# Kernel optimization log

Measured on AMD Instinct MI355X. Metric: run time of the kernel, lower is better.

Reference implementation:

```python
import jax, jax.numpy as jnp
import numpy as np

B, S, DIM, H, HD = 2, 2048, 512, 8, 64
VD = DIM // H  # 64
QK = H * HD


def setup_inputs() -> dict:
    key = jax.random.key(0)
    k1, k2, k3, k4, k5 = jax.random.split(key, 5)
    x = jax.random.normal(k1, (B, S, DIM), dtype=jnp.float32)
    mask = jax.random.bernoulli(k2, 0.5, (B, S))
    # per-position rotation matrices, scaled to keep activations O(1)
    rotator = jax.random.normal(k3, (B, S, HD, HD), dtype=jnp.float32) / np.sqrt(HD)
    # torch Linear weights: [out_features, in_features], no bias
    W_trans = jax.random.normal(k4, (2 * QK + DIM, DIM), dtype=jnp.float32) / np.sqrt(DIM)
    W_o = jax.random.normal(k5, (DIM, DIM), dtype=jnp.float32) / np.sqrt(DIM)
    return {"x": x, "mask": mask, "rotator": rotator, "W_trans": W_trans, "W_o": W_o}


def _taylor_attention(qs, ks, vs, mask):
    # 2nd-order Taylor approximation of exp for softmax weights
    # qs/ks: [B,S,H,HD], vs: [B,S,H,VD], mask: [B,S] key mask
    scores = jnp.einsum('bqhd,bkhd->bhqk', qs, ks) / np.sqrt(HD)
    w = 1.0 + scores + 0.5 * scores * scores
    w = jnp.where(mask[:, None, None, :], w, 0.0)
    w = w / jnp.sum(w, axis=-1, keepdims=True)
    out = jnp.einsum('bhqk,bkhd->bqhd', w, vs)
    return out.reshape(out.shape[0], out.shape[1], -1)  # [B,S,DIM]


def reference(x, mask, rotator, W_trans, W_o):
    t = x @ W_trans.T  # [B,S,2*QK+DIM]
    qs = t[..., :QK].reshape(B, S, H, HD)
    ks = t[..., QK:2 * QK].reshape(B, S, H, HD)
    vs = t[..., 2 * QK:].reshape(B, S, H, VD)
    sel = mask[..., None, None]
    qs = jnp.where(sel, jnp.einsum('bsij,bshj->bshi', rotator, qs), qs)
    ks = jnp.where(sel, jnp.einsum('bsij,bshj->bshi', rotator, ks), ks)
    out = _taylor_attention(qs, ks, vs, mask)
    return out @ W_o.T
```

## Files before the change

### kernel.cpp

```cpp
#include <hip/hip_runtime.h>
#include <hip/hip_bf16.h>

#define B_    2
#define S_    2048
#define DIM_  512
#define H_    8
#define HD_   64
#define TOUT_ 1536
#define ROWS_ (B_ * S_)

typedef unsigned short ushort_t;
typedef __attribute__((ext_vector_type(8))) __bf16 bf16x8;
typedef __attribute__((ext_vector_type(4))) float floatx4;

#define AS_GLB __attribute__((address_space(1)))
#define AS_LDS __attribute__((address_space(3)))

__device__ __forceinline__ float bf2f(unsigned int u) { return __uint_as_float(u << 16); }
__device__ __forceinline__ unsigned short f2bfu(float f) {
    unsigned u = __float_as_uint(f);
    unsigned r = (u + 0x7fffu + ((u >> 16) & 1u)) >> 16;
    return (unsigned short)r;
}
__device__ __forceinline__ bf16x8 cvt8(const float* p) {
    float4 a = *reinterpret_cast<const float4*>(p);
    float4 b = *reinterpret_cast<const float4*>(p + 4);
    ushort_t o[8] = {f2bfu(a.x), f2bfu(a.y), f2bfu(a.z), f2bfu(a.w),
                     f2bfu(b.x), f2bfu(b.y), f2bfu(b.z), f2bfu(b.w)};
    return *reinterpret_cast<bf16x8*>(o);
}

__global__ void tmha_detect(const unsigned char* mb, int* flags) {
    __shared__ int s_bf, s_f, s_u8;
    int tid = threadIdx.x;
    if (tid == 0) { s_bf = 0; s_f = 0; s_u8 = 0; }
    __syncthreads();
    int cbf = 0, cf = 0, cu8 = 0;
    for (int i = tid; i < 4096; i += 256) {
        unsigned char v = mb[i];
        if (v == 0x3F || v == 0x80) {
            cf++;
            if ((i & 3) == 1) cbf++;
        } else if (v != 0 && (i & 3) != 0) {
            cu8++;
        }
    }
    atomicAdd(&s_bf, cbf); atomicAdd(&s_f, cf); atomicAdd(&s_u8, cu8);
    __syncthreads();
    if (tid == 0) {
        int mcls;
        if (s_bf > 0)      mcls = 2;
        else if (s_f > 0)  mcls = 3;
        else if (s_u8 > 0) mcls = 0;
        else               mcls = 1;
        flags[1] = mcls;
    }
}

__global__ void tmha_decode_mask(const unsigned char* mb, const int* flags, int* wm) {
    int i = blockIdx.x * 256 + threadIdx.x;
    if (i >= ROWS_) return;
    int cls = flags[1];
    int v;
    if (cls == 0)      v = (mb[i] != 0);
    else if (cls == 1) v = (reinterpret_cast<const int*>(mb)[i] != 0);
    else if (cls == 2) v = ((reinterpret_cast<const unsigned short*>(mb)[i] & 0x7fffu) != 0);
    else               v = ((reinterpret_cast<const unsigned int*>(mb)[i] & 0x7fffffffu) != 0);
    wm[i] = v;
}

__global__ __launch_bounds__(256) void cast_bf16(const float* __restrict__ src,
                                                 ushort_t* __restrict__ dst, int n4) {
    int i = blockIdx.x * 256 + threadIdx.x;
    if (i >= n4) return;
    float4 v = reinterpret_cast<const float4*>(src)[i];
    ushort_t o[4] = {f2bfu(v.x), f2bfu(v.y), f2bfu(v.z), f2bfu(v.w)};
    reinterpret_cast<uint2*>(dst)[i] = *reinterpret_cast<uint2*>(o);
}

template <int TM, int N, int K, bool OUT_BF16>
__global__ __launch_bounds__(256) void mfma_gemm_bt(const ushort_t* __restrict__ A,
                                                    const ushort_t* __restrict__ Bm,
                                                    void* __restrict__ Cout) {
    constexpr int FM = TM / 32;
    __shared__ __align__(16) ushort_t As[TM * 64];
    __shared__ __align__(16) ushort_t Bs[128 * 64];
    int tid = threadIdx.x;
    int lane = tid & 63;
    int wv = tid >> 6;
    int wm = wv >> 1, wn = wv & 1;
    int quad = lane >> 4;
    int mrow = lane & 15;
    int bx = blockIdx.x;
    int by = blockIdx.y;

    floatx4 acc[FM][4];
#pragma unroll
    for (int i = 0; i < FM; i++)
#pragma unroll
        for (int j = 0; j < 4; j++) acc[i][j] = (floatx4){0.f, 0.f, 0.f, 0.f};

    for (int k0 = 0; k0 < K; k0 += 64) {
#pragma unroll
        for (int t = 0; t < TM / 32; t++) {
            int p = (wv * (TM / 32) + t) * 64 + lane;
            int row = p >> 3, cp = p & 7;
            int gc = cp ^ (row & 7);
            const ushort_t* ga = A + (size_t)(by * TM + row) * K + k0 + gc * 8;
            __builtin_amdgcn_global_load_lds((const AS_GLB unsigned int*)ga,
                                             (AS_LDS unsigned int*)&As[(size_t)(wv * (TM / 32) + t) * 64 * 8],
                                             16, 0, 0);
        }
#pragma unroll
        for (int t = 0; t < 4; t++) {
            int p = (wv * 4 + t) * 64 + lane;
            int row = p >> 3, cp = p & 7;
            int gc = cp ^ (row & 7);
            const ushort_t* gb = Bm + (size_t)(bx * 128 + row) * K + k0 + gc * 8;
            __builtin_amdgcn_global_load_lds((const AS_GLB unsigned int*)gb,
                                             (AS_LDS unsigned int*)&Bs[(size_t)(wv * 4 + t) * 64 * 8],
                                             16, 0, 0);
        }
        __syncthreads();
#pragma unroll
        for (int ks = 0; ks < 64; ks += 32) {
            int c = (ks >> 3) + quad;
            bf16x8 af[FM], bf[4];
#pragma unroll
            for (int i = 0; i < FM; i++) {
                int row = wm * (TM / 2) + i * 16 + mrow;
                int pos = row * 8 + (c ^ (row & 7));
                af[i] = *reinterpret_cast<const bf16x8*>(&As[pos * 8]);
            }
#pragma unroll
            for (int j = 0; j < 4; j++) {
                int row = wn * 64 + j * 16 + mrow;
                int pos = row * 8 + (c ^ (row & 7));
                bf[j] = *reinterpret_cast<const bf16x8*>(&Bs[pos * 8]);
            }
#pragma unroll
            for (int i = 0; i < FM; i++)
#pragma unroll
                for (int j = 0; j < 4; j++)
                    acc[i][j] = __builtin_amdgcn_mfma_f32_16x16x32_bf16(af[i], bf[j], acc[i][j], 0, 0, 0);
        }
        __syncthreads();
    }

    int col0 = bx * 128 + wn * 64 + mrow;
    int row0 = by * TM + wm * (TM / 2) + quad * 4;
    if constexpr (OUT_BF16) {
        ushort_t* C = reinterpret_cast<ushort_t*>(Cout);
#pragma unroll
        for (int i = 0; i < FM; i++)
#pragma unroll
            for (int j = 0; j < 4; j++)
#pragma unroll
                for (int r = 0; r < 4; r++)
                    C[(size_t)(row0 + i * 16 + r) * N + col0 + j * 16] = f2bfu(acc[i][j][r]);
    } else {
        float* C = reinterpret_cast<float*>(Cout);
#pragma unroll
        for (int i = 0; i < FM; i++)
#pragma unroll
            for (int j = 0; j < 4; j++)
#pragma unroll
                for (int r = 0; r < 4; r++)
                    C[(size_t)(row0 + i * 16 + r) * N + col0 + j * 16] = acc[i][j][r];
    }
}

__global__ __launch_bounds__(256) void rot_qk_mfma(const ushort_t* __restrict__ t,
                                                   const float* __restrict__ rotG,
                                                   const int* __restrict__ wm,
                                                   ushort_t* __restrict__ Qb,
                                                   ushort_t* __restrict__ Kb) {
    int lane = threadIdx.x & 63;
    int wv = threadIdx.x >> 6;
    int row = blockIdx.x * 4 + wv;
    int b = row >> 11, s = row & 2047;
    int lm = lane & 15, quad = lane >> 4;
    const ushort_t* trow = t + (size_t)row * TOUT_;

    if (wm[row]) {
        bf16x8 af[2];
#pragma unroll
        for (int kc = 0; kc < 2; kc++)
            af[kc] = *reinterpret_cast<const bf16x8*>(trow + lm * 64 + kc * 32 + quad * 8);

        const float* R = rotG + (size_t)row * 4096;
        floatx4 dacc[4];
#pragma unroll
        for (int nb = 0; nb < 4; nb++) dacc[nb] = (floatx4){0.f, 0.f, 0.f, 0.f};
#pragma unroll
        for (int nb = 0; nb < 4; nb++)
#pragma unroll
            for (int kc = 0; kc < 2; kc++) {
                bf16x8 bfr = cvt8(R + (size_t)(nb * 16 + lm) * 64 + kc * 32 + quad * 8);
                dacc[nb] = __builtin_amdgcn_mfma_f32_16x16x32_bf16(af[kc], bfr, dacc[nb], 0, 0, 0);
            }
#pragma unroll
        for (int nb = 0; nb < 4; nb++)
#pragma unroll
            for (int r = 0; r < 4; r++) {
                int vec = quad * 4 + r;
                int h = vec & 7;
                ushort_t* dst = (vec >= 8 ? Kb : Qb);
                dst[((size_t)(b * 8 + h) * 2048 + s) * 64 + nb * 16 + lm] = f2bfu(dacc[nb][r]);
            }
    } else {
#pragma unroll
        for (int nb = 0; nb < 4; nb++)
#pragma unroll
            for (int r = 0; r < 4; r++) {
                int vec = quad * 4 + r;
                int h = vec & 7;
                ushort_t* dst = (vec >= 8 ? Kb : Qb);
                dst[((size_t)(b * 8 + h) * 2048 + s) * 64 + nb * 16 + lm] = trow[vec * 64 + nb * 16 + lm];
            }
    }
}

__global__ __launch_bounds__(256) void prep_vt(const ushort_t* __restrict__ t,
                                               const int* __restrict__ wm,
                                               ushort_t* __restrict__ VtG) {
    __shared__ ushort_t tile[64][72];
    __shared__ float mrow[64];
    int st = blockIdx.x;
    int bh = blockIdx.y;
    int b = bh >> 3, h = bh & 7;
    int tid = threadIdx.x;
    if (tid < 64) mrow[tid] = wm[b * 2048 + st * 64 + tid] ? 1.0f : 0.0f;
#pragma unroll
    for (int i = 0; i < 2; i++) {
        int q = i * 256 + tid;
        int r = q >> 3, c8 = (q & 7) * 8;
        uint4 v = *reinterpret_cast<const uint4*>(
            t + (size_t)(b * 2048 + st * 64 + r) * TOUT_ + 1024 + h * 64 + c8);
        *reinterpret_cast<uint4*>(&tile[r][c8]) = v;
    }
    __syncthreads();
#pragma unroll
    for (int i = 0; i < 8; i++) {
        int e = i * 256 + tid;
        int d = e >> 5, sl = (e & 31) * 2;
        unsigned u0 = (mrow[sl]     != 0.f) ? (unsigned)tile[sl][d]     : 0u;
        unsigned u1 = (mrow[sl + 1] != 0.f) ? (unsigned)tile[sl + 1][d] : 0u;
        *reinterpret_cast<unsigned int*>(VtG + ((size_t)bh * 65 + d) * 2048 + st * 64 + sl) = u0 | (u1 << 16);
    }
    if (tid < 32) {
        int sl = tid * 2;
        unsigned m0 = mrow[sl]     != 0.f ? 0x3F80u : 0u;
        unsigned m1 = mrow[sl + 1] != 0.f ? 0x3F80u : 0u;
        *reinterpret_cast<unsigned int*>(VtG + ((size_t)bh * 65 + 64) * 2048 + st * 64 + sl) = m0 | (m1 << 16);
    }
}

__global__ __launch_bounds__(256) void tmha_attn_mfma(const ushort_t* __restrict__ Qb,
                                                      const ushort_t* __restrict__ Kb,
                                                      const ushort_t* __restrict__ VtG,
                                                      float* __restrict__ numer,
                                                      float* __restrict__ den) {
    __shared__ __align__(16) ushort_t Ks[512 * 8];
    __shared__ __align__(16) ushort_t Vs[520 * 8];
    __shared__ __align__(16) ushort_t Ps[512 * 8];
    int tid = threadIdx.x;
    int lane = tid & 63;
    int wv = tid >> 6;
    int lm = lane & 15;
    int quad = lane >> 4;
    int qt = blockIdx.x;
    int h = blockIdx.y;
    int z = blockIdx.z;
    int b = z >> 1;
    int ks = z & 1;
    int bh = b * 8 + h;

    bf16x8 qf[2];
    {
        const ushort_t* qp = Qb + ((size_t)bh * 2048 + qt * 64 + wv * 16 + lm) * 64 + quad * 8;
        qf[0] = *reinterpret_cast<const bf16x8*>(qp);
        qf[1] = *reinterpret_cast<const bf16x8*>(qp + 32);
    }

    bf16x8 vzero;
    *reinterpret_cast<uint4*>(&vzero) = (uint4){0u, 0u, 0u, 0u};

    floatx4 oacc[5];
#pragma unroll
    for (int j = 0; j < 5; j++) oacc[j] = (floatx4){0.f, 0.f, 0.f, 0.f};

    for (int kt = ks * 1024; kt < ks * 1024 + 1024; kt += 64) {
#pragma unroll
        for (int t4 = 0; t4 < 2; t4++) {
            int p = (wv * 2 + t4) * 64 + lane;
            int row = p >> 3, cp = p & 7;
            int gc = cp ^ (row & 7);
            const ushort_t* g = Kb + ((size_t)bh * 2048 + kt + row) * 64 + gc * 8;
            __builtin_amdgcn_global_load_lds((const AS_GLB unsigned int*)g,
                                             (AS_LDS unsigned int*)&Ks[(size_t)(wv * 2 + t4) * 64 * 8],
                                             16, 0, 0);
        }
#pragma unroll
        for (int t4 = 0; t4 < 2; t4++) {
            int p = (wv * 2 + t4) * 64 + lane;
            int row = p >> 3, cp = p & 7;
            int gc = cp ^ (row & 7);
            const ushort_t* g = VtG + ((size_t)bh * 65 + row) * 2048 + kt + gc * 8;
            __builtin_amdgcn_global_load_lds((const AS_GLB unsigned int*)g,
                                             (AS_LDS unsigned int*)&Vs[(size_t)(wv * 2 + t4) * 64 * 8],
                                             16, 0, 0);
        }
        if (tid < 8) {
            const ushort_t* g = VtG + ((size_t)bh * 65 + 64) * 2048 + kt + tid * 8;
            __builtin_amdgcn_global_load_lds((const AS_GLB unsigned int*)g,
                                             (AS_LDS unsigned int*)&Vs[512 * 8],
                                             16, 0, 0);
        }
        __syncthreads();

        floatx4 sacc[4];
#pragma unroll
        for (int j = 0; j < 4; j++) sacc[j] = (floatx4){0.f, 0.f, 0.f, 0.f};
#pragma unroll
        for (int j = 0; j < 4; j++) {
            int row = j * 16 + lm;
#pragma unroll
            for (int kc = 0; kc < 2; kc++) {
                int c = kc * 4 + quad;
                int pos = row * 8 + (c ^ (row & 7));
                bf16x8 bk = *reinterpret_cast<const bf16x8*>(&Ks[pos * 8]);
                sacc[j] = __builtin_amdgcn_mfma_f32_16x16x32_bf16(qf[kc], bk, sacc[j], 0, 0, 0);
            }
        }

#pragma unroll
        for (int j = 0; j < 4; j++)
#pragma unroll
            for (int r = 0; r < 4; r++) {
                float s = sacc[j][r];
                float wgt = fmaf(s, fmaf(s, 0.0078125f, 0.125f), 1.0f);
                int m = wv * 16 + quad * 4 + r;
                int col = j * 16 + lm;
                int cw = col >> 3;
                int pos = m * 8 + (cw ^ (m & 7));
                Ps[pos * 8 + (col & 7)] = f2bfu(wgt);
            }
        asm volatile("s_waitcnt lgkmcnt(0)" ::: "memory");

        int qrow_l = wv * 16 + lm;
#pragma unroll
        for (int j = 0; j < 5; j++) {
            int vrow = (j < 4) ? (j * 16 + lm) : 64;
#pragma unroll
            for (int kc = 0; kc < 2; kc++) {
                int c = kc * 4 + quad;
                int ppos = qrow_l * 8 + (c ^ (qrow_l & 7));
                bf16x8 pa = *reinterpret_cast<const bf16x8*>(&Ps[ppos * 8]);
                int vpos = vrow * 8 + (c ^ (vrow & 7));
                bf16x8 vb = *reinterpret_cast<const bf16x8*>(&Vs[vpos * 8]);
                if (j == 4 && lm != 0) vb = vzero;
                oacc[j] = __builtin_amdgcn_mfma_f32_16x16x32_bf16(pa, vb, oacc[j], 0, 0, 0);
            }
        }
        __syncthreads();
    }

#pragma unroll
    for (int j = 0; j < 4; j++)
#pragma unroll
        for (int r = 0; r < 4; r++) {
            int qrow = b * 2048 + qt * 64 + wv * 16 + quad * 4 + r;
            numer[((size_t)ks * ROWS_ + qrow) * DIM_ + h * 64 + j * 16 + lm] = oacc[j][r];
        }
    if (lm == 0) {
#pragma unroll
        for (int r = 0; r < 4; r++) {
            int qrow = b * 2048 + qt * 64 + wv * 16 + quad * 4 + r;
            den[((size_t)ks * ROWS_ + qrow) * 8 + h] = oacc[4][r];
        }
    }
}

__global__ __launch_bounds__(256) void attn_combine(const float* __restrict__ numer,
                                                    const float* __restrict__ den,
                                                    ushort_t* __restrict__ attnAb) {
    int i = blockIdx.x * 256 + threadIdx.x;
    int row = i >> 7;
    int c4 = (i & 127) * 4;
    int h = c4 >> 6;
    float4 n0 = *reinterpret_cast<const float4*>(&numer[(size_t)row * DIM_ + c4]);
    float4 n1 = *reinterpret_cast<const float4*>(&numer[((size_t)ROWS_ + row) * DIM_ + c4]);
    float d = den[(size_t)row * 8 + h] + den[((size_t)ROWS_ + row) * 8 + h];
    float inv = 1.0f / d;
    ushort_t o[4] = {f2bfu((n0.x + n1.x) * inv), f2bfu((n0.y + n1.y) * inv),
                     f2bfu((n0.z + n1.z) * inv), f2bfu((n0.w + n1.w) * inv)};
    *reinterpret_cast<uint2*>(&attnAb[(size_t)row * DIM_ + c4]) = *reinterpret_cast<uint2*>(o);
}

extern "C" void kernel_launch(void* const* d_in, const int* in_sizes, int n_in,
                              void* d_out, int out_size, void* d_ws, size_t ws_size,
                              hipStream_t stream) {
    (void)in_sizes; (void)n_in; (void)out_size; (void)ws_size;
    const float* x    = (const float*)d_in[0];
    const void*  mask = d_in[1];
    const float* rot  = (const float*)d_in[2];
    const float* Wt   = (const float*)d_in[3];
    const float* Wo   = (const float*)d_in[4];

    char* ws = (char*)d_ws;
    int* flags       = (int*)ws;
    int* wmask       = (int*)(ws + 64);
    ushort_t* t      = (ushort_t*)(ws + 32768);
    ushort_t* Xb     = (ushort_t*)(ws + 25198592);
    ushort_t* Wtb    = (ushort_t*)(ws + 29392896);
    ushort_t* Wob    = (ushort_t*)(ws + 30965760);
    ushort_t* Qb     = (ushort_t*)(ws + 31490048);
    ushort_t* Kb     = (ushort_t*)(ws + 35684352);
    ushort_t* VtG    = (ushort_t*)(ws + 39878656);
    ushort_t* attnAb = (ushort_t*)(ws + 44138496);
    float* numer     = (float*)(ws + 32768);
    float* den       = (float*)(ws + 32768 + 16777216);

    tmha_detect<<<1, 256, 0, stream>>>((const unsigned char*)mask, flags);
    tmha_decode_mask<<<16, 256, 0, stream>>>((const unsigned char*)mask, flags, wmask);

    cast_bf16<<<(ROWS_ * DIM_ / 4 + 255) / 256, 256, 0, stream>>>(x, Xb, ROWS_ * DIM_ / 4);
    cast_bf16<<<(TOUT_ * DIM_ / 4 + 255) / 256, 256, 0, stream>>>(Wt, Wtb, TOUT_ * DIM_ / 4);
    cast_bf16<<<(DIM_ * DIM_ / 4 + 255) / 256, 256, 0, stream>>>(Wo, Wob, DIM_ * DIM_ / 4);

    {
        dim3 grid(TOUT_ / 128, ROWS_ / 64);
        mfma_gemm_bt<64, TOUT_, DIM_, true><<<grid, 256, 0, stream>>>(Xb, Wtb, (void*)t);
    }

    rot_qk_mfma<<<ROWS_ / 4, 256, 0, stream>>>(t, rot, wmask, Qb, Kb);

    {
        dim3 grid(32, 16);
        prep_vt<<<grid, 256, 0, stream>>>(t, wmask, VtG);
    }

    {
        dim3 grid(32, 8, 4);
        tmha_attn_mfma<<<grid, 256, 0, stream>>>(Qb, Kb, VtG, numer, den);
    }
    attn_combine<<<(ROWS_ * 128) / 256, 256, 0, stream>>>(numer, den, attnAb);

    {
        dim3 grid(DIM_ / 128, ROWS_ / 64);
        mfma_gemm_bt<64, DIM_, DIM_, false><<<grid, 256, 0, stream>>>(attnAb, Wob, d_out);
    }
}
```

Before: 194.7 us.

## Double-buffer V in attention, register-prefetch K, 128-query tiles, merge small launches

The attention kernel now handles 128 query rows per block, two 16-row m-tiles per wave. K fragments are prefetched straight into registers one tile ahead, and V is double-buffered in LDS, so global loads overlap the MFMA work and there is one barrier per tile instead of two. The mask-detect and mask-decode kernels are merged into one launch, and the three cast kernels into one. The output GEMM switches to 32-row tiles to launch more blocks. The trade-offs are higher register pressure and half as many attention blocks, which could lower occupancy.

```diff
diff --git a/kernel.cpp b/kernel.cpp
--- a/kernel.cpp
+++ b/kernel.cpp
@@ -16,7 +16,6 @@
 #define AS_GLB __attribute__((address_space(1)))
 #define AS_LDS __attribute__((address_space(3)))
 
-__device__ __forceinline__ float bf2f(unsigned int u) { return __uint_as_float(u << 16); }
 __device__ __forceinline__ unsigned short f2bfu(float f) {
     unsigned u = __float_as_uint(f);
     unsigned r = (u + 0x7fffu + ((u >> 16) & 1u)) >> 16;
@@ -30,7 +29,7 @@
     return *reinterpret_cast<bf16x8*>(o);
 }
 
-__global__ void tmha_detect(const unsigned char* mb, int* flags) {
+__global__ void tmha_mask(const unsigned char* mb, int* wm) {
     __shared__ int s_bf, s_f, s_u8;
     int tid = threadIdx.x;
     if (tid == 0) { s_bf = 0; s_f = 0; s_u8 = 0; }
@@ -47,42 +46,41 @@
     }
     atomicAdd(&s_bf, cbf); atomicAdd(&s_f, cf); atomicAdd(&s_u8, cu8);
     __syncthreads();
-    if (tid == 0) {
-        int mcls;
-        if (s_bf > 0)      mcls = 2;
-        else if (s_f > 0)  mcls = 3;
-        else if (s_u8 > 0) mcls = 0;
-        else               mcls = 1;
-        flags[1] = mcls;
-    }
-}
-
-__global__ void tmha_decode_mask(const unsigned char* mb, const int* flags, int* wm) {
+    int cls = (s_bf > 0) ? 2 : (s_f > 0) ? 3 : (s_u8 > 0) ? 0 : 1;
+    for (int i = tid; i < ROWS_; i += 256) {
+        int v;
+        if (cls == 0)      v = (mb[i] != 0);
+        else if (cls == 1) v = (reinterpret_cast<const int*>(mb)[i] != 0);
+        else if (cls == 2) v = ((reinterpret_cast<const unsigned short*>(mb)[i] & 0x7fffu) != 0);
+        else               v = ((reinterpret_cast<const unsigned int*>(mb)[i] & 0x7fffffffu) != 0);
+        wm[i] = v;
+    }
+}
+
+#define XN4_  (ROWS_ * DIM_ / 4)
+#define WTN4_ (TOUT_ * DIM_ / 4)
+#define WON4_ (DIM_ * DIM_ / 4)
+__global__ __launch_bounds__(256) void cast3_bf16(const float* __restrict__ x,
+                                                  const float* __restrict__ wt,
+                                                  const float* __restrict__ wo,
+                                                  ushort_t* __restrict__ xb,
+                                                  ushort_t* __restrict__ wtb,
+                                                  ushort_t* __restrict__ wob) {
     int i = blockIdx.x * 256 + threadIdx.x;
-    if (i >= ROWS_) return;
-    int cls = flags[1];
-    int v;
-    if (cls == 0)      v = (mb[i] != 0);
-    else if (cls == 1) v = (reinterpret_cast<const int*>(mb)[i] != 0);
-    else if (cls == 2) v = ((reinterpret_cast<const unsigned short*>(mb)[i] & 0x7fffu) != 0);
-    else               v = ((reinterpret_cast<const unsigned int*>(mb)[i] & 0x7fffffffu) != 0);
-    wm[i] = v;
-}
-
-__global__ __launch_bounds__(256) void cast_bf16(const float* __restrict__ src,
-                                                 ushort_t* __restrict__ dst, int n4) {
-    int i = blockIdx.x * 256 + threadIdx.x;
-    if (i >= n4) return;
-    float4 v = reinterpret_cast<const float4*>(src)[i];
+    const float* s; ushort_t* d; int off;
+    if (i < XN4_)              { s = x;  d = xb;  off = i; }
+    else if (i < XN4_ + WTN4_) { s = wt; d = wtb; off = i - XN4_; }
+    else                       { s = wo; d = wob; off = i - XN4_ - WTN4_; }
+    float4 v = reinterpret_cast<const float4*>(s)[off];
     ushort_t o[4] = {f2bfu(v.x), f2bfu(v.y), f2bfu(v.z), f2bfu(v.w)};
-    reinterpret_cast<uint2*>(dst)[i] = *reinterpret_cast<uint2*>(o);
+    reinterpret_cast<uint2*>(d)[off] = *reinterpret_cast<uint2*>(o);
 }
 
 template <int TM, int N, int K, bool OUT_BF16>
 __global__ __launch_bounds__(256) void mfma_gemm_bt(const ushort_t* __restrict__ A,
                                                     const ushort_t* __restrict__ Bm,
                                                     void* __restrict__ Cout) {
-    constexpr int FM = TM / 32;
+    constexpr int FM = (TM + 31) / 32;
     __shared__ __align__(16) ushort_t As[TM * 64];
     __shared__ __align__(16) ushort_t Bs[128 * 64];
     int tid = threadIdx.x;
@@ -261,9 +259,8 @@
                                                       const ushort_t* __restrict__ VtG,
                                                       float* __restrict__ numer,
                                                       float* __restrict__ den) {
-    __shared__ __align__(16) ushort_t Ks[512 * 8];
-    __shared__ __align__(16) ushort_t Vs[520 * 8];
-    __shared__ __align__(16) ushort_t Ps[512 * 8];
+    __shared__ __align__(16) ushort_t Vs[2][520 * 8];
+    __shared__ __align__(16) ushort_t Ps[128 * 8 * 8];
     int tid = threadIdx.x;
     int lane = tid & 63;
     int wv = tid >> 6;
@@ -276,108 +273,156 @@
     int ks = z & 1;
     int bh = b * 8 + h;
 
-    bf16x8 qf[2];
-    {
-        const ushort_t* qp = Qb + ((size_t)bh * 2048 + qt * 64 + wv * 16 + lm) * 64 + quad * 8;
-        qf[0] = *reinterpret_cast<const bf16x8*>(qp);
-        qf[1] = *reinterpret_cast<const bf16x8*>(qp + 32);
+    const ushort_t* Kbh = Kb + (size_t)bh * 2048 * 64;
+    const ushort_t* Vbh = VtG + (size_t)bh * 65 * 2048;
+
+    bf16x8 qf[2][2];
+#pragma unroll
+    for (int m = 0; m < 2; m++) {
+        const ushort_t* qp = Qb + ((size_t)bh * 2048 + qt * 128 + wv * 32 + m * 16 + lm) * 64 + quad * 8;
+        qf[m][0] = *reinterpret_cast<const bf16x8*>(qp);
+        qf[m][1] = *reinterpret_cast<const bf16x8*>(qp + 32);
     }
 
     bf16x8 vzero;
     *reinterpret_cast<uint4*>(&vzero) = (uint4){0u, 0u, 0u, 0u};
 
-    floatx4 oacc[5];
-#pragma unroll
-    for (int j = 0; j < 5; j++) oacc[j] = (floatx4){0.f, 0.f, 0.f, 0.f};
-
-    for (int kt = ks * 1024; kt < ks * 1024 + 1024; kt += 64) {
+    floatx4 oacc[2][4];
+    floatx4 dacc[2];
+#pragma unroll
+    for (int m = 0; m < 2; m++) {
+        dacc[m] = (floatx4){0.f, 0.f, 0.f, 0.f};
+#pragma unroll
+        for (int j = 0; j < 4; j++) oacc[m][j] = (floatx4){0.f, 0.f, 0.f, 0.f};
+    }
+
+    auto stageV = [&](int buf, int kt) {
 #pragma unroll
         for (int t4 = 0; t4 < 2; t4++) {
             int p = (wv * 2 + t4) * 64 + lane;
             int row = p >> 3, cp = p & 7;
             int gc = cp ^ (row & 7);
-            const ushort_t* g = Kb + ((size_t)bh * 2048 + kt + row) * 64 + gc * 8;
+            const ushort_t* g = Vbh + (size_t)row * 2048 + kt + gc * 8;
             __builtin_amdgcn_global_load_lds((const AS_GLB unsigned int*)g,
-                                             (AS_LDS unsigned int*)&Ks[(size_t)(wv * 2 + t4) * 64 * 8],
+                                             (AS_LDS unsigned int*)&Vs[buf][(wv * 2 + t4) * 64 * 8],
                                              16, 0, 0);
         }
-#pragma unroll
-        for (int t4 = 0; t4 < 2; t4++) {
-            int p = (wv * 2 + t4) * 64 + lane;
-            int row = p >> 3, cp = p & 7;
-            int gc = cp ^ (row & 7);
-            const ushort_t* g = VtG + ((size_t)bh * 65 + row) * 2048 + kt + gc * 8;
+        if (tid < 8) {
+            const ushort_t* g = Vbh + (size_t)64 * 2048 + kt + tid * 8;
             __builtin_amdgcn_global_load_lds((const AS_GLB unsigned int*)g,
-                                             (AS_LDS unsigned int*)&Vs[(size_t)(wv * 2 + t4) * 64 * 8],
+                                             (AS_LDS unsigned int*)&Vs[buf][512 * 8],
                                              16, 0, 0);
         }
-        if (tid < 8) {
-            const ushort_t* g = VtG + ((size_t)bh * 65 + 64) * 2048 + kt + tid * 8;
-            __builtin_amdgcn_global_load_lds((const AS_GLB unsigned int*)g,
-                                             (AS_LDS unsigned int*)&Vs[512 * 8],
-                                             16, 0, 0);
-        }
+    };
+    auto loadK = [&](bf16x8 (&kr)[4][2], int kt) {
+#pragma unroll
+        for (int j = 0; j < 4; j++)
+#pragma unroll
+            for (int kc = 0; kc < 2; kc++)
+                kr[j][kc] = *reinterpret_cast<const bf16x8*>(
+                    Kbh + (size_t)(kt + j * 16 + lm) * 64 + (kc * 4 + quad) * 8);
+    };
+
+    auto tile = [&](int buf, bf16x8 (&kr)[4][2], bf16x8 (&krn)[4][2], int ktn) {
         __syncthreads();
-
-        floatx4 sacc[4];
-#pragma unroll
-        for (int j = 0; j < 4; j++) sacc[j] = (floatx4){0.f, 0.f, 0.f, 0.f};
+        stageV(buf ^ 1, ktn);
+
+        floatx4 sacc[2][4];
+#pragma unroll
+        for (int m = 0; m < 2; m++)
+#pragma unroll
+            for (int j = 0; j < 4; j++) sacc[m][j] = (floatx4){0.f, 0.f, 0.f, 0.f};
+#pragma unroll
+        for (int j = 0; j < 4; j++)
+#pragma unroll
+            for (int m = 0; m < 2; m++)
+#pragma unroll
+                for (int kc = 0; kc < 2; kc++)
+                    sacc[m][j] = __builtin_amdgcn_mfma_f32_16x16x32_bf16(kr[j][kc], qf[m][kc], sacc[m][j], 0, 0, 0);
+
+        loadK(krn, ktn);
+
+#pragma unroll
+        for (int m = 0; m < 2; m++)
+#pragma unroll
+            for (int j = 0; j < 4; j++) {
+                ushort_t o[4];
+#pragma unroll
+                for (int r = 0; r < 4; r++) {
+                    float s = sacc[m][j][r];
+                    float wgt = fmaf(s, fmaf(s, 0.0078125f, 0.125f), 1.0f);
+                    o[r] = f2bfu(wgt);
+                }
+                int row = wv * 32 + m * 16 + lm;
+                int k0 = j * 16 + quad * 4;
+                int pos = row * 8 + ((k0 >> 3) ^ (row & 7));
+                *reinterpret_cast<uint2*>(&Ps[pos * 8 + (k0 & 7)]) = *reinterpret_cast<const uint2*>(o);
+            }
+        asm volatile("s_waitcnt lgkmcnt(0)" ::: "memory");
+        __builtin_amdgcn_sched_barrier(0);
+
+        bf16x8 pa[2][2];
+#pragma unroll
+        for (int m = 0; m < 2; m++)
+#pragma unroll
+            for (int kc = 0; kc < 2; kc++) {
+                int row = wv * 32 + m * 16 + lm;
+                int c = kc * 4 + quad;
+                int pos = row * 8 + (c ^ (row & 7));
+                pa[m][kc] = *reinterpret_cast<const bf16x8*>(&Ps[pos * 8]);
+            }
 #pragma unroll
         for (int j = 0; j < 4; j++) {
-            int row = j * 16 + lm;
+            int vrow = j * 16 + lm;
 #pragma unroll
             for (int kc = 0; kc < 2; kc++) {
                 int c = kc * 4 + quad;
-                int pos = row * 8 + (c ^ (row & 7));
-                bf16x8 bk = *reinterpret_cast<const bf16x8*>(&Ks[pos * 8]);
-                sacc[j] = __builtin_amdgcn_mfma_f32_16x16x32_bf16(qf[kc], bk, sacc[j], 0, 0, 0);
-            }
-        }
-
+                int vpos = vrow * 8 + (c ^ (vrow & 7));
+                bf16x8 vb = *reinterpret_cast<const bf16x8*>(&Vs[buf][vpos * 8]);
+#pragma unroll
+                for (int m = 0; m < 2; m++)
+                    oacc[m][j] = __builtin_amdgcn_mfma_f32_16x16x32_bf16(pa[m][kc], vb, oacc[m][j], 0, 0, 0);
+            }
+        }
+#pragma unroll
+        for (int kc = 0; kc < 2; kc++) {
+            int c = kc * 4 + quad;
+            bf16x8 vb = *reinterpret_cast<const bf16x8*>(&Vs[buf][(512 + c) * 8]);
+            if (lm != 0) vb = vzero;
+#pragma unroll
+            for (int m = 0; m < 2; m++)
+                dacc[m] = __builtin_amdgcn_mfma_f32_16x16x32_bf16(pa[m][kc], vb, dacc[m], 0, 0, 0);
+        }
+    };
+
+    bf16x8 kA[4][2], kB[4][2];
+    int kt0 = ks * 1024;
+    stageV(0, kt0);
+    loadK(kA, kt0);
+#pragma unroll 1
+    for (int tt = 0; tt < 8; tt++) {
+        int kt = kt0 + tt * 128;
+        int kt1 = kt + 64;
+        int kt2 = (tt == 7) ? kt0 : kt + 128;
+        tile(0, kA, kB, kt1);
+        tile(1, kB, kA, kt2);
+    }
+
+#pragma unroll
+    for (int m = 0; m < 2; m++) {
 #pragma unroll
         for (int j = 0; j < 4; j++)
 #pragma unroll
             for (int r = 0; r < 4; r++) {
-                float s = sacc[j][r];
-                float wgt = fmaf(s, fmaf(s, 0.0078125f, 0.125f), 1.0f);
-                int m = wv * 16 + quad * 4 + r;
-                int col = j * 16 + lm;
-                int cw = col >> 3;
-                int pos = m * 8 + (cw ^ (m & 7));
-                Ps[pos * 8 + (col & 7)] = f2bfu(wgt);
-            }
-        asm volatile("s_waitcnt lgkmcnt(0)" ::: "memory");
-
-        int qrow_l = wv * 16 + lm;
-#pragma unroll
-        for (int j = 0; j < 5; j++) {
-            int vrow = (j < 4) ? (j * 16 + lm) : 64;
-#pragma unroll
-            for (int kc = 0; kc < 2; kc++) {
-                int c = kc * 4 + quad;
-                int ppos = qrow_l * 8 + (c ^ (qrow_l & 7));
-                bf16x8 pa = *reinterpret_cast<const bf16x8*>(&Ps[ppos * 8]);
-                int vpos = vrow * 8 + (c ^ (vrow & 7));
-                bf16x8 vb = *reinterpret_cast<const bf16x8*>(&Vs[vpos * 8]);
-                if (j == 4 && lm != 0) vb = vzero;
-                oacc[j] = __builtin_amdgcn_mfma_f32_16x16x32_bf16(pa, vb, oacc[j], 0, 0, 0);
-            }
-        }
-        __syncthreads();
-    }
-
-#pragma unroll
-    for (int j = 0; j < 4; j++)
-#pragma unroll
-        for (int r = 0; r < 4; r++) {
-            int qrow = b * 2048 + qt * 64 + wv * 16 + quad * 4 + r;
-            numer[((size_t)ks * ROWS_ + qrow) * DIM_ + h * 64 + j * 16 + lm] = oacc[j][r];
-        }
-    if (lm == 0) {
-#pragma unroll
-        for (int r = 0; r < 4; r++) {
-            int qrow = b * 2048 + qt * 64 + wv * 16 + quad * 4 + r;
-            den[((size_t)ks * ROWS_ + qrow) * 8 + h] = oacc[4][r];
+                int qrow = b * 2048 + qt * 128 + wv * 32 + m * 16 + quad * 4 + r;
+                numer[((size_t)ks * ROWS_ + qrow) * DIM_ + h * 64 + j * 16 + lm] = oacc[m][j][r];
+            }
+        if (lm == 0) {
+#pragma unroll
+            for (int r = 0; r < 4; r++) {
+                int qrow = b * 2048 + qt * 128 + wv * 32 + m * 16 + quad * 4 + r;
+                den[((size_t)ks * ROWS_ + qrow) * 8 + h] = dacc[m][r];
+            }
         }
     }
 }
@@ -409,7 +454,6 @@
     const float* Wo   = (const float*)d_in[4];
 
     char* ws = (char*)d_ws;
-    int* flags       = (int*)ws;
     int* wmask       = (int*)(ws + 64);
     ushort_t* t      = (ushort_t*)(ws + 32768);
     ushort_t* Xb     = (ushort_t*)(ws + 25198592);
@@ -422,12 +466,9 @@
     float* numer     = (float*)(ws + 32768);
     float* den       = (float*)(ws + 32768 + 16777216);
 
-    tmha_detect<<<1, 256, 0, stream>>>((const unsigned char*)mask, flags);
-    tmha_decode_mask<<<16, 256, 0, stream>>>((const unsigned char*)mask, flags, wmask);
-
-    cast_bf16<<<(ROWS_ * DIM_ / 4 + 255) / 256, 256, 0, stream>>>(x, Xb, ROWS_ * DIM_ / 4);
-    cast_bf16<<<(TOUT_ * DIM_ / 4 + 255) / 256, 256, 0, stream>>>(Wt, Wtb, TOUT_ * DIM_ / 4);
-    cast_bf16<<<(DIM_ * DIM_ / 4 + 255) / 256, 256, 0, stream>>>(Wo, Wob, DIM_ * DIM_ / 4);
+    tmha_mask<<<1, 256, 0, stream>>>((const unsigned char*)mask, wmask);
+
+    cast3_bf16<<<(XN4_ + WTN4_ + WON4_) / 256, 256, 0, stream>>>(x, Wt, Wo, Xb, Wtb, Wob);
 
     {
         dim3 grid(TOUT_ / 128, ROWS_ / 64);
@@ -442,13 +483,13 @@
     }
 
     {
-        dim3 grid(32, 8, 4);
+        dim3 grid(16, 8, 4);
         tmha_attn_mfma<<<grid, 256, 0, stream>>>(Qb, Kb, VtG, numer, den);
     }
     attn_combine<<<(ROWS_ * 128) / 256, 256, 0, stream>>>(numer, den, attnAb);
 
     {
-        dim3 grid(DIM_ / 128, ROWS_ / 64);
-        mfma_gemm_bt<64, DIM_, DIM_, false><<<grid, 256, 0, stream>>>(attnAb, Wob, d_out);
-    }
-}
+        dim3 grid(DIM_ / 128, ROWS_ / 32);
+        mfma_gemm_bt<32, DIM_, DIM_, false><<<grid, 256, 0, stream>>>(attnAb, Wob, d_out);
+    }
+}
```

After: 208.0 us. 1.07x slower.

## Fuse prep kernels, load K fragments directly, double-buffer V in attention

Applied to the files above, without the earlier changes.

Merges mask detection and decoding into one kernel and the three fp32-to-bf16 casts into one launch, cutting launch overhead. Stores K in an MFMA-fragment-friendly blocked layout so the attention kernel loads K straight into registers instead of going through LDS. The V tile is double-buffered with prefetch of the next tile, which removes one barrier per iteration. Output GEMM uses a 32-row tile to launch more blocks. This adds register pressure and a new coupled K layout between kernels.

```diff
diff --git a/kernel.cpp b/kernel.cpp
--- a/kernel.cpp
+++ b/kernel.cpp
@@ -16,7 +16,6 @@
 #define AS_GLB __attribute__((address_space(1)))
 #define AS_LDS __attribute__((address_space(3)))
 
-__device__ __forceinline__ float bf2f(unsigned int u) { return __uint_as_float(u << 16); }
 __device__ __forceinline__ unsigned short f2bfu(float f) {
     unsigned u = __float_as_uint(f);
     unsigned r = (u + 0x7fffu + ((u >> 16) & 1u)) >> 16;
@@ -30,7 +29,7 @@
     return *reinterpret_cast<bf16x8*>(o);
 }
 
-__global__ void tmha_detect(const unsigned char* mb, int* flags) {
+__global__ void tmha_mask(const unsigned char* mb, int* wm) {
     __shared__ int s_bf, s_f, s_u8;
     int tid = threadIdx.x;
     if (tid == 0) { s_bf = 0; s_f = 0; s_u8 = 0; }
@@ -47,42 +46,41 @@
     }
     atomicAdd(&s_bf, cbf); atomicAdd(&s_f, cf); atomicAdd(&s_u8, cu8);
     __syncthreads();
-    if (tid == 0) {
-        int mcls;
-        if (s_bf > 0)      mcls = 2;
-        else if (s_f > 0)  mcls = 3;
-        else if (s_u8 > 0) mcls = 0;
-        else               mcls = 1;
-        flags[1] = mcls;
-    }
-}
-
-__global__ void tmha_decode_mask(const unsigned char* mb, const int* flags, int* wm) {
+    int cls = (s_bf > 0) ? 2 : (s_f > 0) ? 3 : (s_u8 > 0) ? 0 : 1;
+    for (int i = tid; i < ROWS_; i += 256) {
+        int v;
+        if (cls == 0)      v = (mb[i] != 0);
+        else if (cls == 1) v = (reinterpret_cast<const int*>(mb)[i] != 0);
+        else if (cls == 2) v = ((reinterpret_cast<const unsigned short*>(mb)[i] & 0x7fffu) != 0);
+        else               v = ((reinterpret_cast<const unsigned int*>(mb)[i] & 0x7fffffffu) != 0);
+        wm[i] = v;
+    }
+}
+
+#define XN4_  (ROWS_ * DIM_ / 4)
+#define WTN4_ (TOUT_ * DIM_ / 4)
+#define WON4_ (DIM_ * DIM_ / 4)
+__global__ __launch_bounds__(256) void cast3_bf16(const float* __restrict__ x,
+                                                  const float* __restrict__ wt,
+                                                  const float* __restrict__ wo,
+                                                  ushort_t* __restrict__ xb,
+                                                  ushort_t* __restrict__ wtb,
+                                                  ushort_t* __restrict__ wob) {
     int i = blockIdx.x * 256 + threadIdx.x;
-    if (i >= ROWS_) return;
-    int cls = flags[1];
-    int v;
-    if (cls == 0)      v = (mb[i] != 0);
-    else if (cls == 1) v = (reinterpret_cast<const int*>(mb)[i] != 0);
-    else if (cls == 2) v = ((reinterpret_cast<const unsigned short*>(mb)[i] & 0x7fffu) != 0);
-    else               v = ((reinterpret_cast<const unsigned int*>(mb)[i] & 0x7fffffffu) != 0);
-    wm[i] = v;
-}
-
-__global__ __launch_bounds__(256) void cast_bf16(const float* __restrict__ src,
-                                                 ushort_t* __restrict__ dst, int n4) {
-    int i = blockIdx.x * 256 + threadIdx.x;
-    if (i >= n4) return;
-    float4 v = reinterpret_cast<const float4*>(src)[i];
+    const float* s; ushort_t* d; int off;
+    if (i < XN4_)              { s = x;  d = xb;  off = i; }
+    else if (i < XN4_ + WTN4_) { s = wt; d = wtb; off = i - XN4_; }
+    else                       { s = wo; d = wob; off = i - XN4_ - WTN4_; }
+    float4 v = reinterpret_cast<const float4*>(s)[off];
     ushort_t o[4] = {f2bfu(v.x), f2bfu(v.y), f2bfu(v.z), f2bfu(v.w)};
-    reinterpret_cast<uint2*>(dst)[i] = *reinterpret_cast<uint2*>(o);
+    reinterpret_cast<uint2*>(d)[off] = *reinterpret_cast<uint2*>(o);
 }
 
 template <int TM, int N, int K, bool OUT_BF16>
 __global__ __launch_bounds__(256) void mfma_gemm_bt(const ushort_t* __restrict__ A,
                                                     const ushort_t* __restrict__ Bm,
                                                     void* __restrict__ Cout) {
-    constexpr int FM = TM / 32;
+    constexpr int FM = (TM + 31) / 32;
     __shared__ __align__(16) ushort_t As[TM * 64];
     __shared__ __align__(16) ushort_t Bs[128 * 64];
     int tid = threadIdx.x;
@@ -181,6 +179,7 @@
     int b = row >> 11, s = row & 2047;
     int lm = lane & 15, quad = lane >> 4;
     const ushort_t* trow = t + (size_t)row * TOUT_;
+    int kb = s >> 4, l = s & 15;
 
     if (wm[row]) {
         bf16x8 af[2];
@@ -204,9 +203,14 @@
 #pragma unroll
             for (int r = 0; r < 4; r++) {
                 int vec = quad * 4 + r;
-                int h = vec & 7;
-                ushort_t* dst = (vec >= 8 ? Kb : Qb);
-                dst[((size_t)(b * 8 + h) * 2048 + s) * 64 + nb * 16 + lm] = f2bfu(dacc[nb][r]);
+                int hh = vec & 7;
+                ushort_t v = f2bfu(dacc[nb][r]);
+                if (vec >= 8) {
+                    int c = nb * 2 + (lm >> 3), e = lm & 7;
+                    Kb[(((size_t)(b * 8 + hh) * 128 + kb) * 8 + c) * 128 + l * 8 + e] = v;
+                } else {
+                    Qb[((size_t)(b * 8 + hh) * 2048 + s) * 64 + nb * 16 + lm] = v;
+                }
             }
     } else {
 #pragma unroll
@@ -214,9 +218,14 @@
 #pragma unroll
             for (int r = 0; r < 4; r++) {
                 int vec = quad * 4 + r;
-                int h = vec & 7;
-                ushort_t* dst = (vec >= 8 ? Kb : Qb);
-                dst[((size_t)(b * 8 + h) * 2048 + s) * 64 + nb * 16 + lm] = trow[vec * 64 + nb * 16 + lm];
+                int hh = vec & 7;
+                ushort_t v = trow[vec * 64 + nb * 16 + lm];
+                if (vec >= 8) {
+                    int c = nb * 2 + (lm >> 3), e = lm & 7;
+                    Kb[(((size_t)(b * 8 + hh) * 128 + kb) * 8 + c) * 128 + l * 8 + e] = v;
+                } else {
+                    Qb[((size_t)(b * 8 + hh) * 2048 + s) * 64 + nb * 16 + lm] = v;
+                }
             }
     }
 }
@@ -257,12 +266,11 @@
 }
 
 __global__ __launch_bounds__(256) void tmha_attn_mfma(const ushort_t* __restrict__ Qb,
-                                                      const ushort_t* __restrict__ Kb,
+                                                      const ushort_t* __restrict__ KbF,
                                                       const ushort_t* __restrict__ VtG,
                                                       float* __restrict__ numer,
                                                       float* __restrict__ den) {
-    __shared__ __align__(16) ushort_t Ks[512 * 8];
-    __shared__ __align__(16) ushort_t Vs[520 * 8];
+    __shared__ __align__(16) ushort_t Vs[2][520 * 8];
     __shared__ __align__(16) ushort_t Ps[512 * 8];
     int tid = threadIdx.x;
     int lane = tid & 63;
@@ -276,6 +284,9 @@
     int ks = z & 1;
     int bh = b * 8 + h;
 
+    const ushort_t* Kf  = KbF + (size_t)bh * 128 * 1024;
+    const ushort_t* Vbh = VtG + (size_t)bh * 65 * 2048;
+
     bf16x8 qf[2];
     {
         const ushort_t* qp = Qb + ((size_t)bh * 2048 + qt * 64 + wv * 16 + lm) * 64 + quad * 8;
@@ -290,49 +301,55 @@
 #pragma unroll
     for (int j = 0; j < 5; j++) oacc[j] = (floatx4){0.f, 0.f, 0.f, 0.f};
 
-    for (int kt = ks * 1024; kt < ks * 1024 + 1024; kt += 64) {
+    bf16x8 kr[4][2];
+    auto loadK = [&](int kt) {
+        int kb = kt >> 4;
+#pragma unroll
+        for (int j = 0; j < 4; j++)
+#pragma unroll
+            for (int kc = 0; kc < 2; kc++)
+                kr[j][kc] = *reinterpret_cast<const bf16x8*>(
+                    Kf + (((size_t)(kb + j) * 8 + kc * 4 + quad) * 16 + lm) * 8);
+    };
+    auto stageV = [&](int buf, int kt) {
 #pragma unroll
         for (int t4 = 0; t4 < 2; t4++) {
             int p = (wv * 2 + t4) * 64 + lane;
             int row = p >> 3, cp = p & 7;
             int gc = cp ^ (row & 7);
-            const ushort_t* g = Kb + ((size_t)bh * 2048 + kt + row) * 64 + gc * 8;
+            const ushort_t* g = Vbh + (size_t)row * 2048 + kt + gc * 8;
             __builtin_amdgcn_global_load_lds((const AS_GLB unsigned int*)g,
-                                             (AS_LDS unsigned int*)&Ks[(size_t)(wv * 2 + t4) * 64 * 8],
+                                             (AS_LDS unsigned int*)&Vs[buf][(wv * 2 + t4) * 64 * 8],
                                              16, 0, 0);
         }
-#pragma unroll
-        for (int t4 = 0; t4 < 2; t4++) {
-            int p = (wv * 2 + t4) * 64 + lane;
-            int row = p >> 3, cp = p & 7;
-            int gc = cp ^ (row & 7);
-            const ushort_t* g = VtG + ((size_t)bh * 65 + row) * 2048 + kt + gc * 8;
+        if (tid < 8) {
+            const ushort_t* g = Vbh + (size_t)64 * 2048 + kt + tid * 8;
             __builtin_amdgcn_global_load_lds((const AS_GLB unsigned int*)g,
-                                             (AS_LDS unsigned int*)&Vs[(size_t)(wv * 2 + t4) * 64 * 8],
+                                             (AS_LDS unsigned int*)&Vs[buf][512 * 8],
                                              16, 0, 0);
         }
-        if (tid < 8) {
-            const ushort_t* g = VtG + ((size_t)bh * 65 + 64) * 2048 + kt + tid * 8;
-            __builtin_amdgcn_global_load_lds((const AS_GLB unsigned int*)g,
-                                             (AS_LDS unsigned int*)&Vs[512 * 8],
-                                             16, 0, 0);
-        }
+    };
+
+    int kt0 = ks * 1024;
+    stageV(0, kt0);
+    loadK(kt0);
+    int buf = 0;
+#pragma unroll 1
+    for (int tt = 0; tt < 16; tt++) {
+        int ktn = (tt == 15) ? kt0 : kt0 + (tt + 1) * 64;
         __syncthreads();
+        stageV(buf ^ 1, ktn);
 
         floatx4 sacc[4];
 #pragma unroll
         for (int j = 0; j < 4; j++) sacc[j] = (floatx4){0.f, 0.f, 0.f, 0.f};
 #pragma unroll
-        for (int j = 0; j < 4; j++) {
-            int row = j * 16 + lm;
-#pragma unroll
-            for (int kc = 0; kc < 2; kc++) {
-                int c = kc * 4 + quad;
-                int pos = row * 8 + (c ^ (row & 7));
-                bf16x8 bk = *reinterpret_cast<const bf16x8*>(&Ks[pos * 8]);
-                sacc[j] = __builtin_amdgcn_mfma_f32_16x16x32_bf16(qf[kc], bk, sacc[j], 0, 0, 0);
-            }
-        }
+        for (int j = 0; j < 4; j++)
+#pragma unroll
+            for (int kc = 0; kc < 2; kc++)
+                sacc[j] = __builtin_amdgcn_mfma_f32_16x16x32_bf16(qf[kc], kr[j][kc], sacc[j], 0, 0, 0);
+
+        loadK(ktn);
 
 #pragma unroll
         for (int j = 0; j < 4; j++)
@@ -347,23 +364,29 @@
                 Ps[pos * 8 + (col & 7)] = f2bfu(wgt);
             }
         asm volatile("s_waitcnt lgkmcnt(0)" ::: "memory");
+        __builtin_amdgcn_sched_barrier(0);
 
         int qrow_l = wv * 16 + lm;
+        bf16x8 pa[2];
+#pragma unroll
+        for (int kc = 0; kc < 2; kc++) {
+            int c = kc * 4 + quad;
+            int ppos = qrow_l * 8 + (c ^ (qrow_l & 7));
+            pa[kc] = *reinterpret_cast<const bf16x8*>(&Ps[ppos * 8]);
+        }
 #pragma unroll
         for (int j = 0; j < 5; j++) {
             int vrow = (j < 4) ? (j * 16 + lm) : 64;
 #pragma unroll
             for (int kc = 0; kc < 2; kc++) {
                 int c = kc * 4 + quad;
-                int ppos = qrow_l * 8 + (c ^ (qrow_l & 7));
-                bf16x8 pa = *reinterpret_cast<const bf16x8*>(&Ps[ppos * 8]);
                 int vpos = vrow * 8 + (c ^ (vrow & 7));
-                bf16x8 vb = *reinterpret_cast<const bf16x8*>(&Vs[vpos * 8]);
+                bf16x8 vb = *reinterpret_cast<const bf16x8*>(&Vs[buf][vpos * 8]);
                 if (j == 4 && lm != 0) vb = vzero;
-                oacc[j] = __builtin_amdgcn_mfma_f32_16x16x32_bf16(pa, vb, oacc[j], 0, 0, 0);
-            }
-        }
-        __syncthreads();
+                oacc[j] = __builtin_amdgcn_mfma_f32_16x16x32_bf16(pa[kc], vb, oacc[j], 0, 0, 0);
+            }
+        }
+        buf ^= 1;
     }
 
 #pragma unroll
@@ -409,7 +432,6 @@
     const float* Wo   = (const float*)d_in[4];
 
     char* ws = (char*)d_ws;
-    int* flags       = (int*)ws;
     int* wmask       = (int*)(ws + 64);
     ushort_t* t      = (ushort_t*)(ws + 32768);
     ushort_t* Xb     = (ushort_t*)(ws + 25198592);
@@ -422,12 +444,9 @@
     float* numer     = (float*)(ws + 32768);
     float* den       = (float*)(ws + 32768 + 16777216);
 
-    tmha_detect<<<1, 256, 0, stream>>>((const unsigned char*)mask, flags);
-    tmha_decode_mask<<<16, 256, 0, stream>>>((const unsigned char*)mask, flags, wmask);
-
-    cast_bf16<<<(ROWS_ * DIM_ / 4 + 255) / 256, 256, 0, stream>>>(x, Xb, ROWS_ * DIM_ / 4);
-    cast_bf16<<<(TOUT_ * DIM_ / 4 + 255) / 256, 256, 0, stream>>>(Wt, Wtb, TOUT_ * DIM_ / 4);
-    cast_bf16<<<(DIM_ * DIM_ / 4 + 255) / 256, 256, 0, stream>>>(Wo, Wob, DIM_ * DIM_ / 4);
+    tmha_mask<<<1, 256, 0, stream>>>((const unsigned char*)mask, wmask);
+
+    cast3_bf16<<<(XN4_ + WTN4_ + WON4_) / 256, 256, 0, stream>>>(x, Wt, Wo, Xb, Wtb, Wob);
 
     {
         dim3 grid(TOUT_ / 128, ROWS_ / 64);
@@ -448,7 +467,7 @@
     attn_combine<<<(ROWS_ * 128) / 256, 256, 0, stream>>>(numer, den, attnAb);
 
     {
-        dim3 grid(DIM_ / 128, ROWS_ / 64);
-        mfma_gemm_bt<64, DIM_, DIM_, false><<<grid, 256, 0, stream>>>(attnAb, Wob, d_out);
-    }
-}
+        dim3 grid(DIM_ / 128, ROWS_ / 32);
+        mfma_gemm_bt<32, DIM_, DIM_, false><<<grid, 256, 0, stream>>>(attnAb, Wob, d_out);
+    }
+}
```

Measured after the change: 194.0 us. No clear change (-0.4%).
